# Optimization experiments

Measured on AMD Instinct MI355X. Metric: run time of the kernel, lower is better.

The kernel has to match this reference:

```python
import jax, jax.numpy as jnp
import numpy as np

B, T, I, H, S = 4096, 512, 4, 32, 4


def setup_inputs() -> dict:
    key = jax.random.key(0)
    ks = jax.random.split(key, 8)
    sc_ih = 1.0 / np.sqrt(H)
    return {
        "x": jax.random.normal(ks[0], (B, T, I), dtype=jnp.float32),
        "h0": jnp.zeros((1, B, H), dtype=jnp.float32),
        # PyTorch GRU params: weight_ih_l0 [3H, I] (r,z,n order), weight_hh_l0 [3H, H], biases [3H]
        "w_ih": jax.random.uniform(ks[1], (3 * H, I), jnp.float32, -sc_ih, sc_ih),
        "w_hh": jax.random.uniform(ks[2], (3 * H, H), jnp.float32, -sc_ih, sc_ih),
        "b_ih": jax.random.uniform(ks[3], (3 * H,), jnp.float32, -sc_ih, sc_ih),
        "b_hh": jax.random.uniform(ks[4], (3 * H,), jnp.float32, -sc_ih, sc_ih),
        "w_proj": jax.random.uniform(ks[5], (S, H), jnp.float32, -sc_ih, sc_ih),
        "b_proj": jax.random.uniform(ks[6], (S,), jnp.float32, -sc_ih, sc_ih),
    }


def _gru(x, h0, w_ih, w_hh, b_ih, b_hh):
    # Precompute input contributions for all timesteps: [B, T, 3H]
    xg = jnp.einsum('bti,gi->btg', x, w_ih) + b_ih
    xg_t = jnp.transpose(xg, (1, 0, 2))  # [T, B, 3H]
    h = h0[0]  # [B, H] (num_layers == 1)
    Hdim = w_hh.shape[1]

    def step(h, xg_step):
        hg = h @ w_hh.T + b_hh  # [B, 3H]
        xr, xz, xn = jnp.split(xg_step, 3, axis=-1)
        hr, hz, hn = jnp.split(hg, 3, axis=-1)
        r = jax.nn.sigmoid(xr + hr)
        z = jax.nn.sigmoid(xz + hz)
        n = jnp.tanh(xn + r * hn)
        h_new = (1.0 - z) * n + z * h
        return h_new, h_new

    hT, outs = jax.lax.scan(step, h, xg_t)
    out = jnp.transpose(outs, (1, 0, 2))  # [B, T, H]
    return out, hT[None]  # hn: [1, B, H]


def reference(x, h0, w_ih, w_hh, b_ih, b_hh, w_proj, b_proj):
    out, hn = _gru(x, h0, w_ih, w_hh, b_ih, b_hh)
    state = jnp.einsum('bth,sh->bts', out, w_proj) + b_proj  # [B, T, S]
    return state, hn
```

## Files before the change

kernel.cpp:

```cpp
#include <hip/hip_runtime.h>
#include <stdint.h>

#define BB 4096
#define TT 512
#define II 4
#define HH 32
#define SS 4

__device__ __forceinline__ float fast_sigm(float a) {
  return __builtin_amdgcn_rcpf(1.0f + __expf(-a));
}
__device__ __forceinline__ float fast_tanh(float y) {
  return 1.0f - 2.0f * __builtin_amdgcn_rcpf(__expf(2.0f * y) + 1.0f);
}

__global__ __launch_bounds__(256, 2) void gru_kernel(
    const float* __restrict__ x, const float* __restrict__ h0,
    const float* __restrict__ w_ih, const float* __restrict__ w_hh,
    const float* __restrict__ b_ih, const float* __restrict__ b_hh,
    const float* __restrict__ w_proj, const float* __restrict__ b_proj,
    float* __restrict__ out) {
  const int tid  = threadIdx.x;
  const int wid  = tid >> 6;
  const int lane = tid & 63;
  const int g    = lane >> 5;
  const int j    = lane & 31;
  const int row  = wid * 2 + g;
  const int b    = blockIdx.x * 8 + row;

  __shared__ float lds_h[8][36];
  float* lrow = &lds_h[row][0];

  const float4* whh4 = (const float4*)w_hh;
  float4 wr[8], wz[8], wn[8];
#pragma unroll
  for (int c = 0; c < 8; ++c) {
    wr[c] = whh4[(0 * HH + j) * 8 + c];
    wz[c] = whh4[(1 * HH + j) * 8 + c];
    wn[c] = whh4[(2 * HH + j) * 8 + c];
  }
  const float4* wih4 = (const float4*)w_ih;
  const float4 wir = wih4[0 * HH + j];
  const float4 wiz = wih4[1 * HH + j];
  const float4 win = wih4[2 * HH + j];
  const float bir = b_ih[0 * HH + j], biz = b_ih[1 * HH + j], bin_ = b_ih[2 * HH + j];
  const float bhr = b_hh[0 * HH + j], bhz = b_hh[1 * HH + j], bhn = b_hh[2 * HH + j];

  const int s_idx = j & 3;
  const int c_idx = j >> 2;
  const float4* wp4 = (const float4*)w_proj;
  const float4 wp = wp4[s_idx * 8 + c_idx];
  const float bp = b_proj[s_idx];

  float h_self = h0[(size_t)b * HH + j];
  lrow[j] = h_self;

  const float4* xp = (const float4*)(x + (size_t)b * TT * II);
  float* outp = out + (size_t)b * TT * SS;

  float4 xv = xp[0];

  for (int t = 0; t < TT; ++t) {
    float4 xvn = xp[(t + 1 < TT) ? (t + 1) : t];

    float4 ha[8];
#pragma unroll
    for (int c = 0; c < 8; ++c) ha[c] = *(const float4*)&lrow[c * 4];

    float xr = fmaf(wir.x, xv.x, fmaf(wir.y, xv.y, fmaf(wir.z, xv.z, fmaf(wir.w, xv.w, bir))));
    float xz = fmaf(wiz.x, xv.x, fmaf(wiz.y, xv.y, fmaf(wiz.z, xv.z, fmaf(wiz.w, xv.w, biz))));
    float xn = fmaf(win.x, xv.x, fmaf(win.y, xv.y, fmaf(win.z, xv.z, fmaf(win.w, xv.w, bin_))));

    float hr = bhr, hz = bhz, hn = bhn;
#pragma unroll
    for (int c = 0; c < 8; ++c) {
      hr = fmaf(wr[c].x, ha[c].x, hr); hr = fmaf(wr[c].y, ha[c].y, hr);
      hr = fmaf(wr[c].z, ha[c].z, hr); hr = fmaf(wr[c].w, ha[c].w, hr);
      hz = fmaf(wz[c].x, ha[c].x, hz); hz = fmaf(wz[c].y, ha[c].y, hz);
      hz = fmaf(wz[c].z, ha[c].z, hz); hz = fmaf(wz[c].w, ha[c].w, hz);
      hn = fmaf(wn[c].x, ha[c].x, hn); hn = fmaf(wn[c].y, ha[c].y, hn);
      hn = fmaf(wn[c].z, ha[c].z, hn); hn = fmaf(wn[c].w, ha[c].w, hn);
    }

    const float r  = fast_sigm(xr + hr);
    const float zz = fast_sigm(xz + hz);
    const float nn = fast_tanh(fmaf(r, hn, xn));
    const float hnew = fmaf(zz, h_self - nn, nn);
    h_self = hnew;

    lrow[j] = hnew;

    const float4 hc = *(const float4*)&lrow[c_idx * 4];
    float v = fmaf(wp.x, hc.x, fmaf(wp.y, hc.y, fmaf(wp.z, hc.z, wp.w * hc.w)));
    v += __shfl_xor(v, 4, 64);
    v += __shfl_xor(v, 8, 64);
    v += __shfl_xor(v, 16, 64);
    if (c_idx == 0) {
      outp[t * SS + s_idx] = v + bp;
    }

    xv = xvn;
  }

  out[(size_t)BB * TT * SS + (size_t)b * HH + j] = h_self;
}

extern "C" void kernel_launch(void* const* d_in, const int* in_sizes, int n_in,
                              void* d_out, int out_size, void* d_ws, size_t ws_size,
                              hipStream_t stream) {
  const float* x      = (const float*)d_in[0];
  const float* h0     = (const float*)d_in[1];
  const float* w_ih   = (const float*)d_in[2];
  const float* w_hh   = (const float*)d_in[3];
  const float* b_ih   = (const float*)d_in[4];
  const float* b_hh   = (const float*)d_in[5];
  const float* w_proj = (const float*)d_in[6];
  const float* b_proj = (const float*)d_in[7];
  float* out = (float*)d_out;

  dim3 grid(BB / 8), block(256);
  hipLaunchKernelGGL(gru_kernel, grid, block, 0, stream,
                     x, h0, w_ih, w_hh, b_ih, b_hh, w_proj, b_proj, out);
}
```

Baseline: 332.5 us.

## Split GRU hidden dot product across wave halves with packed FMA

Each wavefront now handles one batch row instead of two. Each half-wave computes half of the 32-wide recurrent dot product using v_pk_fma_f32, and the halves are combined with a cross-half shuffle. This halves the per-thread weight registers and serial FMA chain, and launch bounds rise to 4 blocks per CU for more occupancy. The projection output is moved to the start of the next iteration so it overlaps with the recurrence. The trade-off is twice as many blocks and redundant gate math in both halves.

Result: slower. 361.1 us (+8.6%).

```diff
diff --git a/kernel.cpp b/kernel.cpp
--- a/kernel.cpp
+++ b/kernel.cpp
@@ -3,9 +3,10 @@
 
 #define BB 4096
 #define TT 512
-#define II 4
 #define HH 32
 #define SS 4
+
+typedef float v2f __attribute__((ext_vector_type(2)));
 
 __device__ __forceinline__ float fast_sigm(float a) {
   return __builtin_amdgcn_rcpf(1.0f + __expf(-a));
@@ -13,8 +14,12 @@
 __device__ __forceinline__ float fast_tanh(float y) {
   return 1.0f - 2.0f * __builtin_amdgcn_rcpf(__expf(2.0f * y) + 1.0f);
 }
+__device__ __forceinline__ v2f pkfma(v2f a, v2f b, v2f c) {
+  asm("v_pk_fma_f32 %0, %1, %2, %0" : "+v"(c) : "v"(a), "v"(b));
+  return c;
+}
 
-__global__ __launch_bounds__(256, 2) void gru_kernel(
+__global__ __launch_bounds__(256, 4) void gru_kernel(
     const float* __restrict__ x, const float* __restrict__ h0,
     const float* __restrict__ w_ih, const float* __restrict__ w_hh,
     const float* __restrict__ b_ih, const float* __restrict__ b_hh,
@@ -23,28 +28,36 @@
   const int tid  = threadIdx.x;
   const int wid  = tid >> 6;
   const int lane = tid & 63;
-  const int g    = lane >> 5;
   const int j    = lane & 31;
-  const int row  = wid * 2 + g;
-  const int b    = blockIdx.x * 8 + row;
+  const int half = lane >> 5;
+  const int b    = blockIdx.x * 4 + wid;
 
-  __shared__ float lds_h[8][36];
-  float* lrow = &lds_h[row][0];
+  __shared__ float lds_h[4][36];
+  float* lrow = &lds_h[wid][0];
 
   const float4* whh4 = (const float4*)w_hh;
-  float4 wr[8], wz[8], wn[8];
+  v2f wr2[8], wz2[8], wn2[8];
 #pragma unroll
-  for (int c = 0; c < 8; ++c) {
-    wr[c] = whh4[(0 * HH + j) * 8 + c];
-    wz[c] = whh4[(1 * HH + j) * 8 + c];
-    wn[c] = whh4[(2 * HH + j) * 8 + c];
+  for (int c = 0; c < 4; ++c) {
+    float4 q;
+    q = whh4[(0 * HH + j) * 8 + half * 4 + c];
+    wr2[2*c] = (v2f){q.x, q.y}; wr2[2*c+1] = (v2f){q.z, q.w};
+    q = whh4[(1 * HH + j) * 8 + half * 4 + c];
+    wz2[2*c] = (v2f){q.x, q.y}; wz2[2*c+1] = (v2f){q.z, q.w};
+    q = whh4[(2 * HH + j) * 8 + half * 4 + c];
+    wn2[2*c] = (v2f){q.x, q.y}; wn2[2*c+1] = (v2f){q.z, q.w};
   }
+#pragma unroll
+  for (int m = 0; m < 8; ++m) {
+    asm("" : "+v"(wr2[m]), "+v"(wz2[m]), "+v"(wn2[m]));
+  }
+
   const float4* wih4 = (const float4*)w_ih;
   const float4 wir = wih4[0 * HH + j];
   const float4 wiz = wih4[1 * HH + j];
   const float4 win = wih4[2 * HH + j];
-  const float bir = b_ih[0 * HH + j], biz = b_ih[1 * HH + j], bin_ = b_ih[2 * HH + j];
-  const float bhr = b_hh[0 * HH + j], bhz = b_hh[1 * HH + j], bhn = b_hh[2 * HH + j];
+  const float bir = b_ih[0*HH + j], biz = b_ih[1*HH + j], bin_ = b_ih[2*HH + j];
+  const float bhr = b_hh[0*HH + j], bhz = b_hh[1*HH + j], bhn = b_hh[2*HH + j];
 
   const int s_idx = j & 3;
   const int c_idx = j >> 2;
@@ -55,32 +68,49 @@
   float h_self = h0[(size_t)b * HH + j];
   lrow[j] = h_self;
 
-  const float4* xp = (const float4*)(x + (size_t)b * TT * II);
+  const float4* xp = (const float4*)(x + (size_t)b * TT * 4);
   float* outp = out + (size_t)b * TT * SS;
+  const float* hk_addr = lrow + half * 16;
+  const float* hc_addr = lrow + (c_idx << 2);
 
-  float4 xv = xp[0];
+  for (int t = 0; t <= TT; ++t) {
+    v2f h2[8];
+#pragma unroll
+    for (int c = 0; c < 4; ++c) {
+      const float4 q = *(const float4*)(hk_addr + 4 * c);
+      h2[2*c] = (v2f){q.x, q.y}; h2[2*c+1] = (v2f){q.z, q.w};
+    }
+    const float4 hcv = *(const float4*)hc_addr;
 
-  for (int t = 0; t < TT; ++t) {
-    float4 xvn = xp[(t + 1 < TT) ? (t + 1) : t];
+    if (t > 0) {
+      float v = fmaf(wp.x, hcv.x, fmaf(wp.y, hcv.y,
+                fmaf(wp.z, hcv.z, wp.w * hcv.w)));
+      v += __shfl_xor(v, 4, 64);
+      v += __shfl_xor(v, 8, 64);
+      v += __shfl_xor(v, 16, 64);
+      if (lane < 4) {
+        outp[(t - 1) * SS + lane] = v + bp;
+      }
+    }
+    if (t == TT) break;
 
-    float4 ha[8];
-#pragma unroll
-    for (int c = 0; c < 8; ++c) ha[c] = *(const float4*)&lrow[c * 4];
+    const float4 xv = xp[t];
 
     float xr = fmaf(wir.x, xv.x, fmaf(wir.y, xv.y, fmaf(wir.z, xv.z, fmaf(wir.w, xv.w, bir))));
     float xz = fmaf(wiz.x, xv.x, fmaf(wiz.y, xv.y, fmaf(wiz.z, xv.z, fmaf(wiz.w, xv.w, biz))));
     float xn = fmaf(win.x, xv.x, fmaf(win.y, xv.y, fmaf(win.z, xv.z, fmaf(win.w, xv.w, bin_))));
 
-    float hr = bhr, hz = bhz, hn = bhn;
+    v2f aR = (v2f){0.f, 0.f}, aZ = (v2f){0.f, 0.f}, aN = (v2f){0.f, 0.f};
 #pragma unroll
-    for (int c = 0; c < 8; ++c) {
-      hr = fmaf(wr[c].x, ha[c].x, hr); hr = fmaf(wr[c].y, ha[c].y, hr);
-      hr = fmaf(wr[c].z, ha[c].z, hr); hr = fmaf(wr[c].w, ha[c].w, hr);
-      hz = fmaf(wz[c].x, ha[c].x, hz); hz = fmaf(wz[c].y, ha[c].y, hz);
-      hz = fmaf(wz[c].z, ha[c].z, hz); hz = fmaf(wz[c].w, ha[c].w, hz);
-      hn = fmaf(wn[c].x, ha[c].x, hn); hn = fmaf(wn[c].y, ha[c].y, hn);
-      hn = fmaf(wn[c].z, ha[c].z, hn); hn = fmaf(wn[c].w, ha[c].w, hn);
+    for (int m = 0; m < 8; ++m) {
+      aR = pkfma(wr2[m], h2[m], aR);
+      aZ = pkfma(wz2[m], h2[m], aZ);
+      aN = pkfma(wn2[m], h2[m], aN);
     }
+    float hrp = aR.x + aR.y, hzp = aZ.x + aZ.y, hnp = aN.x + aN.y;
+    const float hr = hrp + __shfl_xor(hrp, 32, 64) + bhr;
+    const float hz = hzp + __shfl_xor(hzp, 32, 64) + bhz;
+    const float hn = hnp + __shfl_xor(hnp, 32, 64) + bhn;
 
     const float r  = fast_sigm(xr + hr);
     const float zz = fast_sigm(xz + hz);
@@ -89,20 +119,11 @@
     h_self = hnew;
 
     lrow[j] = hnew;
-
-    const float4 hc = *(const float4*)&lrow[c_idx * 4];
-    float v = fmaf(wp.x, hc.x, fmaf(wp.y, hc.y, fmaf(wp.z, hc.z, wp.w * hc.w)));
-    v += __shfl_xor(v, 4, 64);
-    v += __shfl_xor(v, 8, 64);
-    v += __shfl_xor(v, 16, 64);
-    if (c_idx == 0) {
-      outp[t * SS + s_idx] = v + bp;
-    }
-
-    xv = xvn;
   }
 
-  out[(size_t)BB * TT * SS + (size_t)b * HH + j] = h_self;
+  if (half == 0) {
+    out[(size_t)BB * TT * SS + (size_t)b * HH + j] = h_self;
+  }
 }
 
 extern "C" void kernel_launch(void* const* d_in, const int* in_sizes, int n_in,
@@ -118,7 +139,7 @@
   const float* b_proj = (const float*)d_in[7];
   float* out = (float*)d_out;
 
-  dim3 grid(BB / 8), block(256);
+  dim3 grid(BB / 4), block(256);
   hipLaunchKernelGGL(gru_kernel, grid, block, 0, stream,
                      x, h0, w_ih, w_hh, b_ih, b_hh, w_proj, b_proj, out);
 }
```

## Use packed FMA for hidden matvec and defer projection by one step

Applied to the files above, without the earlier changes.

Replaces the scalar FMA chains in the recurrent matvec with v_pk_fma_f32 on float pairs, which halves the FMA instruction count and splits each dot product into two accumulators. The projection of h_t is moved to the start of the next iteration so it shares the LDS read of the hidden state and sits off the recurrence's critical path. Weights are loaded with inline-asm global loads behind a single wait. The inline asm and sched barrier may constrain compiler scheduling, and the loop gains one extra iteration.

After: 291.9 us. 12.2% less time.

```diff
diff --git a/kernel.cpp b/kernel.cpp
--- a/kernel.cpp
+++ b/kernel.cpp
@@ -3,15 +3,29 @@
 
 #define BB 4096
 #define TT 512
-#define II 4
 #define HH 32
 #define SS 4
+
+typedef float v2f __attribute__((ext_vector_type(2)));
+
+#define STR2(x) #x
+#define STR(x) STR2(x)
+#define GLOAD4(dst, ptr, off)                                                  \
+  asm volatile("global_load_dwordx4 %0, %1, off offset:" STR(off)              \
+               : "=v"(dst) : "v"(ptr))
+#define GLOAD1(dst, ptr, off)                                                  \
+  asm volatile("global_load_dword %0, %1, off offset:" STR(off)                \
+               : "=v"(dst) : "v"(ptr))
 
 __device__ __forceinline__ float fast_sigm(float a) {
   return __builtin_amdgcn_rcpf(1.0f + __expf(-a));
 }
 __device__ __forceinline__ float fast_tanh(float y) {
   return 1.0f - 2.0f * __builtin_amdgcn_rcpf(__expf(2.0f * y) + 1.0f);
+}
+__device__ __forceinline__ v2f pkfma(v2f a, v2f b, v2f c) {
+  asm("v_pk_fma_f32 %0, %1, %2, %0" : "+v"(c) : "v"(a), "v"(b));
+  return c;
 }
 
 __global__ __launch_bounds__(256, 2) void gru_kernel(
@@ -31,56 +45,97 @@
   __shared__ float lds_h[8][36];
   float* lrow = &lds_h[row][0];
 
-  const float4* whh4 = (const float4*)w_hh;
-  float4 wr[8], wz[8], wn[8];
+  const int s_idx = j & 3;
+  const int c_idx = j >> 2;
+
+  float4 wq[24];
+  float4 wih_r, wih_z, wih_n;
+  float4 wp;
+  float bir, biz, bin_, bhr, bhz, bhn, bp;
+  {
+    const char* p0 = (const char*)(w_hh + (0 * HH + j) * HH);
+    const char* p1 = (const char*)(w_hh + (1 * HH + j) * HH);
+    const char* p2 = (const char*)(w_hh + (2 * HH + j) * HH);
+    GLOAD4(wq[0],  p0, 0);  GLOAD4(wq[1],  p0, 16);
+    GLOAD4(wq[2],  p0, 32); GLOAD4(wq[3],  p0, 48);
+    GLOAD4(wq[4],  p0, 64); GLOAD4(wq[5],  p0, 80);
+    GLOAD4(wq[6],  p0, 96); GLOAD4(wq[7],  p0, 112);
+    GLOAD4(wq[8],  p1, 0);  GLOAD4(wq[9],  p1, 16);
+    GLOAD4(wq[10], p1, 32); GLOAD4(wq[11], p1, 48);
+    GLOAD4(wq[12], p1, 64); GLOAD4(wq[13], p1, 80);
+    GLOAD4(wq[14], p1, 96); GLOAD4(wq[15], p1, 112);
+    GLOAD4(wq[16], p2, 0);  GLOAD4(wq[17], p2, 16);
+    GLOAD4(wq[18], p2, 32); GLOAD4(wq[19], p2, 48);
+    GLOAD4(wq[20], p2, 64); GLOAD4(wq[21], p2, 80);
+    GLOAD4(wq[22], p2, 96); GLOAD4(wq[23], p2, 112);
+    const char* pi = (const char*)(w_ih + j * 4);
+    GLOAD4(wih_r, pi, 0); GLOAD4(wih_z, pi, 512); GLOAD4(wih_n, pi, 1024);
+    const char* pbi = (const char*)(b_ih + j);
+    GLOAD1(bir, pbi, 0); GLOAD1(biz, pbi, 128); GLOAD1(bin_, pbi, 256);
+    const char* pbh = (const char*)(b_hh + j);
+    GLOAD1(bhr, pbh, 0); GLOAD1(bhz, pbh, 128); GLOAD1(bhn, pbh, 256);
+    const char* pp = (const char*)(w_proj + (s_idx * 8 + c_idx) * 4);
+    GLOAD4(wp, pp, 0);
+    const char* pbp = (const char*)(b_proj + s_idx);
+    GLOAD1(bp, pbp, 0);
+    asm volatile("s_waitcnt vmcnt(0)" ::: "memory");
+    __builtin_amdgcn_sched_barrier(0);
+  }
+
+  v2f wr2[16], wz2[16], wn2[16];
 #pragma unroll
   for (int c = 0; c < 8; ++c) {
-    wr[c] = whh4[(0 * HH + j) * 8 + c];
-    wz[c] = whh4[(1 * HH + j) * 8 + c];
-    wn[c] = whh4[(2 * HH + j) * 8 + c];
+    wr2[2*c] = (v2f){wq[c].x,    wq[c].y};    wr2[2*c+1] = (v2f){wq[c].z,    wq[c].w};
+    wz2[2*c] = (v2f){wq[8+c].x,  wq[8+c].y};  wz2[2*c+1] = (v2f){wq[8+c].z,  wq[8+c].w};
+    wn2[2*c] = (v2f){wq[16+c].x, wq[16+c].y}; wn2[2*c+1] = (v2f){wq[16+c].z, wq[16+c].w};
   }
-  const float4* wih4 = (const float4*)w_ih;
-  const float4 wir = wih4[0 * HH + j];
-  const float4 wiz = wih4[1 * HH + j];
-  const float4 win = wih4[2 * HH + j];
-  const float bir = b_ih[0 * HH + j], biz = b_ih[1 * HH + j], bin_ = b_ih[2 * HH + j];
-  const float bhr = b_hh[0 * HH + j], bhz = b_hh[1 * HH + j], bhn = b_hh[2 * HH + j];
-
-  const int s_idx = j & 3;
-  const int c_idx = j >> 2;
-  const float4* wp4 = (const float4*)w_proj;
-  const float4 wp = wp4[s_idx * 8 + c_idx];
-  const float bp = b_proj[s_idx];
 
   float h_self = h0[(size_t)b * HH + j];
   lrow[j] = h_self;
 
-  const float4* xp = (const float4*)(x + (size_t)b * TT * II);
+  const float4* xp = (const float4*)(x + (size_t)b * TT * 4);
   float* outp = out + (size_t)b * TT * SS;
+  const float* hc_addr = lrow + (c_idx << 2);
 
   float4 xv = xp[0];
 
-  for (int t = 0; t < TT; ++t) {
+  for (int t = 0; t <= TT; ++t) {
+    v2f h2[16];
+#pragma unroll
+    for (int c = 0; c < 8; ++c) {
+      const float4 q = *(const float4*)(lrow + 4 * c);
+      h2[2*c] = (v2f){q.x, q.y}; h2[2*c+1] = (v2f){q.z, q.w};
+    }
+    const float4 hcv = *(const float4*)hc_addr;
+
+    if (t > 0) {
+      float v = fmaf(wp.x, hcv.x, fmaf(wp.y, hcv.y,
+                fmaf(wp.z, hcv.z, wp.w * hcv.w)));
+      v += __shfl_xor(v, 4, 64);
+      v += __shfl_xor(v, 8, 64);
+      v += __shfl_xor(v, 16, 64);
+      if (c_idx == 0) {
+        outp[(t - 1) * SS + s_idx] = v + bp;
+      }
+    }
+    if (t == TT) break;
+
     float4 xvn = xp[(t + 1 < TT) ? (t + 1) : t];
 
-    float4 ha[8];
+    float xr = fmaf(wih_r.x, xv.x, fmaf(wih_r.y, xv.y, fmaf(wih_r.z, xv.z, fmaf(wih_r.w, xv.w, bir))));
+    float xz = fmaf(wih_z.x, xv.x, fmaf(wih_z.y, xv.y, fmaf(wih_z.z, xv.z, fmaf(wih_z.w, xv.w, biz))));
+    float xn = fmaf(wih_n.x, xv.x, fmaf(wih_n.y, xv.y, fmaf(wih_n.z, xv.z, fmaf(wih_n.w, xv.w, bin_))));
+
+    v2f aR = (v2f){bhr, 0.f}, aZ = (v2f){bhz, 0.f}, aN = (v2f){bhn, 0.f};
 #pragma unroll
-    for (int c = 0; c < 8; ++c) ha[c] = *(const float4*)&lrow[c * 4];
-
-    float xr = fmaf(wir.x, xv.x, fmaf(wir.y, xv.y, fmaf(wir.z, xv.z, fmaf(wir.w, xv.w, bir))));
-    float xz = fmaf(wiz.x, xv.x, fmaf(wiz.y, xv.y, fmaf(wiz.z, xv.z, fmaf(wiz.w, xv.w, biz))));
-    float xn = fmaf(win.x, xv.x, fmaf(win.y, xv.y, fmaf(win.z, xv.z, fmaf(win.w, xv.w, bin_))));
-
-    float hr = bhr, hz = bhz, hn = bhn;
-#pragma unroll
-    for (int c = 0; c < 8; ++c) {
-      hr = fmaf(wr[c].x, ha[c].x, hr); hr = fmaf(wr[c].y, ha[c].y, hr);
-      hr = fmaf(wr[c].z, ha[c].z, hr); hr = fmaf(wr[c].w, ha[c].w, hr);
-      hz = fmaf(wz[c].x, ha[c].x, hz); hz = fmaf(wz[c].y, ha[c].y, hz);
-      hz = fmaf(wz[c].z, ha[c].z, hz); hz = fmaf(wz[c].w, ha[c].w, hz);
-      hn = fmaf(wn[c].x, ha[c].x, hn); hn = fmaf(wn[c].y, ha[c].y, hn);
-      hn = fmaf(wn[c].z, ha[c].z, hn); hn = fmaf(wn[c].w, ha[c].w, hn);
+    for (int m = 0; m < 16; ++m) {
+      aR = pkfma(wr2[m], h2[m], aR);
+      aZ = pkfma(wz2[m], h2[m], aZ);
+      aN = pkfma(wn2[m], h2[m], aN);
     }
+    const float hr = aR.x + aR.y;
+    const float hz = aZ.x + aZ.y;
+    const float hn = aN.x + aN.y;
 
     const float r  = fast_sigm(xr + hr);
     const float zz = fast_sigm(xz + hz);
@@ -89,15 +144,6 @@
     h_self = hnew;
 
     lrow[j] = hnew;
-
-    const float4 hc = *(const float4*)&lrow[c_idx * 4];
-    float v = fmaf(wp.x, hc.x, fmaf(wp.y, hc.y, fmaf(wp.z, hc.z, wp.w * hc.w)));
-    v += __shfl_xor(v, 4, 64);
-    v += __shfl_xor(v, 8, 64);
-    v += __shfl_xor(v, 16, 64);
-    if (c_idx == 0) {
-      outp[t * SS + s_idx] = v + bp;
-    }
 
     xv = xvn;
   }
```

## Compute GRU recurrent matmul with bf16 MFMA using hi/lo split of hidden state

Applied to the files above, without the earlier changes.

Each 64-lane block now processes 16 batch rows and computes the hidden-to-hidden gates and the output projection with 16x16x32 bf16 MFMA instructions. The hidden state is split into a high and a low bf16 part so precision stays close to fp32, while the weights are rounded to bf16 only once. This replaces the per-lane 96-FMA scalar dot products and the shuffle reduction for the projection. It also double-buffers x in LDS and delays each projection store by one step. The cost is more MFMA issue per step and bf16 rounding error in the weights.

Result: slower. 476.2 us (+43.2%).

```diff
diff --git a/kernel.cpp b/kernel.cpp
--- a/kernel.cpp
+++ b/kernel.cpp
@@ -3,106 +3,184 @@
 
 #define BB 4096
 #define TT 512
-#define II 4
 #define HH 32
 #define SS 4
 
+typedef __attribute__((ext_vector_type(8))) short bf16x8;
+typedef __attribute__((ext_vector_type(4))) float f32x4;
+
+union Frag { uint32_t u[4]; bf16x8 v; };
+
+__device__ __forceinline__ uint32_t cvtpk(float a, float b) {
+  uint32_t d;
+  asm("v_cvt_pk_bf16_f32 %0, %1, %2" : "=v"(d) : "v"(a), "v"(b));
+  return d;
+}
+__device__ __forceinline__ float bflo(uint32_t u) { return __uint_as_float(u << 16); }
+__device__ __forceinline__ float bfhi(uint32_t u) { return __uint_as_float(u & 0xFFFF0000u); }
+
 __device__ __forceinline__ float fast_sigm(float a) {
   return __builtin_amdgcn_rcpf(1.0f + __expf(-a));
 }
 __device__ __forceinline__ float fast_tanh(float y) {
   return 1.0f - 2.0f * __builtin_amdgcn_rcpf(__expf(2.0f * y) + 1.0f);
 }
-
-__global__ __launch_bounds__(256, 2) void gru_kernel(
-    const float* __restrict__ x, const float* __restrict__ h0,
-    const float* __restrict__ w_ih, const float* __restrict__ w_hh,
-    const float* __restrict__ b_ih, const float* __restrict__ b_hh,
-    const float* __restrict__ w_proj, const float* __restrict__ b_proj,
-    float* __restrict__ out) {
-  const int tid  = threadIdx.x;
-  const int wid  = tid >> 6;
-  const int lane = tid & 63;
-  const int g    = lane >> 5;
-  const int j    = lane & 31;
-  const int row  = wid * 2 + g;
-  const int b    = blockIdx.x * 8 + row;
-
-  __shared__ float lds_h[8][36];
-  float* lrow = &lds_h[row][0];
-
-  const float4* whh4 = (const float4*)w_hh;
-  float4 wr[8], wz[8], wn[8];
-#pragma unroll
-  for (int c = 0; c < 8; ++c) {
-    wr[c] = whh4[(0 * HH + j) * 8 + c];
-    wz[c] = whh4[(1 * HH + j) * 8 + c];
-    wn[c] = whh4[(2 * HH + j) * 8 + c];
-  }
+__device__ __forceinline__ float dot4(float4 w, float4 x, float init) {
+  return fmaf(w.x, x.x, fmaf(w.y, x.y, fmaf(w.z, x.z, fmaf(w.w, x.w, init))));
+}
+
+#define MFMA(acc, afrag, bfrag) \
+  acc = __builtin_amdgcn_mfma_f32_16x16x32_bf16((afrag).v, (bfrag).v, acc, 0, 0, 0)
+
+#define MKB(frag, grow)                                                        \
+  { const float4* p_ = (const float4*)(w_hh + (size_t)(grow) * HH + k0);       \
+    float4 p0_ = p_[0], p1_ = p_[1];                                           \
+    (frag).u[0] = cvtpk(p0_.x, p0_.y); (frag).u[1] = cvtpk(p0_.z, p0_.w);      \
+    (frag).u[2] = cvtpk(p1_.x, p1_.y); (frag).u[3] = cvtpk(p1_.z, p1_.w); }
+
+__global__ void __attribute__((amdgpu_flat_work_group_size(64, 64)))
+__attribute__((amdgpu_waves_per_eu(1, 4)))
+gru_kernel(const float* __restrict__ x, const float* __restrict__ h0,
+           const float* __restrict__ w_ih, const float* __restrict__ w_hh,
+           const float* __restrict__ b_ih, const float* __restrict__ b_hh,
+           const float* __restrict__ w_proj, const float* __restrict__ b_proj,
+           float* __restrict__ out) {
+  const int lane = threadIdx.x;
+  const int c    = lane & 15;
+  const int qh   = lane >> 4;
+  const int k0   = qh * 8;
+  const int b0   = blockIdx.x * 16;
+
+  __shared__ float  hbuf[16][36];
+  __shared__ float4 xs[2][16];
+
+  {
+    const float4* hp = (const float4*)(h0 + (size_t)(b0 + c) * HH + k0);
+    float4 a0 = hp[0], a1 = hp[1];
+    *(float4*)&hbuf[c][k0]     = a0;
+    *(float4*)&hbuf[c][k0 + 4] = a1;
+  }
+  if (lane < 16) {
+    xs[0][lane] = *(const float4*)(x + (size_t)(b0 + lane) * TT * 4);
+  }
+
   const float4* wih4 = (const float4*)w_ih;
-  const float4 wir = wih4[0 * HH + j];
-  const float4 wiz = wih4[1 * HH + j];
-  const float4 win = wih4[2 * HH + j];
-  const float bir = b_ih[0 * HH + j], biz = b_ih[1 * HH + j], bin_ = b_ih[2 * HH + j];
-  const float bhr = b_hh[0 * HH + j], bhz = b_hh[1 * HH + j], bhn = b_hh[2 * HH + j];
-
-  const int s_idx = j & 3;
-  const int c_idx = j >> 2;
-  const float4* wp4 = (const float4*)w_proj;
-  const float4 wp = wp4[s_idx * 8 + c_idx];
-  const float bp = b_proj[s_idx];
-
-  float h_self = h0[(size_t)b * HH + j];
-  lrow[j] = h_self;
-
-  const float4* xp = (const float4*)(x + (size_t)b * TT * II);
-  float* outp = out + (size_t)b * TT * SS;
-
-  float4 xv = xp[0];
+  const float4 wr_c = wih4[c],      wr_d = wih4[16 + c];
+  const float4 wz_c = wih4[32 + c], wz_d = wih4[48 + c];
+  const float4 wn_c = wih4[64 + c], wn_d = wih4[80 + c];
+
+  const float bsr0 = b_ih[c]      + b_hh[c];
+  const float bsr1 = b_ih[16 + c] + b_hh[16 + c];
+  const float bsz0 = b_ih[32 + c] + b_hh[32 + c];
+  const float bsz1 = b_ih[48 + c] + b_hh[48 + c];
+  const float bin0 = b_ih[64 + c], bin1 = b_ih[80 + c];
+  const float bhn0 = b_hh[64 + c], bhn1 = b_hh[80 + c];
+  const float bp   = b_proj[c & 3];
+
+  Frag br0, br1, bz0, bz1, bn0, bn1, bpr;
+  MKB(br0, c);       MKB(br1, 16 + c);
+  MKB(bz0, 32 + c);  MKB(bz1, 48 + c);
+  MKB(bn0, 64 + c);  MKB(bn1, 80 + c);
+  if (c < 4) {
+    const float4* p = (const float4*)(w_proj + (size_t)c * HH + k0);
+    float4 p0 = p[0], p1 = p[1];
+    bpr.u[0] = cvtpk(p0.x, p0.y); bpr.u[1] = cvtpk(p0.z, p0.w);
+    bpr.u[2] = cvtpk(p1.x, p1.y); bpr.u[3] = cvtpk(p1.z, p1.w);
+  } else {
+    bpr.u[0] = 0; bpr.u[1] = 0; bpr.u[2] = 0; bpr.u[3] = 0;
+  }
 
   for (int t = 0; t < TT; ++t) {
-    float4 xvn = xp[(t + 1 < TT) ? (t + 1) : t];
-
-    float4 ha[8];
-#pragma unroll
-    for (int c = 0; c < 8; ++c) ha[c] = *(const float4*)&lrow[c * 4];
-
-    float xr = fmaf(wir.x, xv.x, fmaf(wir.y, xv.y, fmaf(wir.z, xv.z, fmaf(wir.w, xv.w, bir))));
-    float xz = fmaf(wiz.x, xv.x, fmaf(wiz.y, xv.y, fmaf(wiz.z, xv.z, fmaf(wiz.w, xv.w, biz))));
-    float xn = fmaf(win.x, xv.x, fmaf(win.y, xv.y, fmaf(win.z, xv.z, fmaf(win.w, xv.w, bin_))));
-
-    float hr = bhr, hz = bhz, hn = bhn;
-#pragma unroll
-    for (int c = 0; c < 8; ++c) {
-      hr = fmaf(wr[c].x, ha[c].x, hr); hr = fmaf(wr[c].y, ha[c].y, hr);
-      hr = fmaf(wr[c].z, ha[c].z, hr); hr = fmaf(wr[c].w, ha[c].w, hr);
-      hz = fmaf(wz[c].x, ha[c].x, hz); hz = fmaf(wz[c].y, ha[c].y, hz);
-      hz = fmaf(wz[c].z, ha[c].z, hz); hz = fmaf(wz[c].w, ha[c].w, hz);
-      hn = fmaf(wn[c].x, ha[c].x, hn); hn = fmaf(wn[c].y, ha[c].y, hn);
-      hn = fmaf(wn[c].z, ha[c].z, hn); hn = fmaf(wn[c].w, ha[c].w, hn);
-    }
-
-    const float r  = fast_sigm(xr + hr);
-    const float zz = fast_sigm(xz + hz);
-    const float nn = fast_tanh(fmaf(r, hn, xn));
-    const float hnew = fmaf(zz, h_self - nn, nn);
-    h_self = hnew;
-
-    lrow[j] = hnew;
-
-    const float4 hc = *(const float4*)&lrow[c_idx * 4];
-    float v = fmaf(wp.x, hc.x, fmaf(wp.y, hc.y, fmaf(wp.z, hc.z, wp.w * hc.w)));
-    v += __shfl_xor(v, 4, 64);
-    v += __shfl_xor(v, 8, 64);
-    v += __shfl_xor(v, 16, 64);
-    if (c_idx == 0) {
-      outp[t * SS + s_idx] = v + bp;
-    }
-
-    xv = xvn;
-  }
-
-  out[(size_t)BB * TT * SS + (size_t)b * HH + j] = h_self;
+    const int tn = (t + 1 < TT) ? (t + 1) : t;
+    float4 xpre;
+    if (lane < 16) {
+      xpre = *(const float4*)(x + (size_t)(b0 + lane) * TT * 4 + (size_t)tn * 4);
+    }
+
+    const float4 q0 = *(const float4*)&hbuf[c][k0];
+    const float4 q1 = *(const float4*)&hbuf[c][k0 + 4];
+    Frag ahi, alo;
+    ahi.u[0] = cvtpk(q0.x, q0.y); ahi.u[1] = cvtpk(q0.z, q0.w);
+    ahi.u[2] = cvtpk(q1.x, q1.y); ahi.u[3] = cvtpk(q1.z, q1.w);
+    alo.u[0] = cvtpk(q0.x - bflo(ahi.u[0]), q0.y - bfhi(ahi.u[0]));
+    alo.u[1] = cvtpk(q0.z - bflo(ahi.u[1]), q0.w - bfhi(ahi.u[1]));
+    alo.u[2] = cvtpk(q1.x - bflo(ahi.u[2]), q1.y - bfhi(ahi.u[2]));
+    alo.u[3] = cvtpk(q1.z - bflo(ahi.u[3]), q1.w - bfhi(ahi.u[3]));
+
+    f32x4 ar0, ar1, az0, az1, an0, an1, ap;
+    float xn0[4], xn1[4], hold0[4], hold1[4];
+#pragma unroll
+    for (int i = 0; i < 4; ++i) {
+      const int m = qh * 4 + i;
+      const float4 xv = xs[t & 1][m];
+      ar0[i] = dot4(wr_c, xv, bsr0);
+      ar1[i] = dot4(wr_d, xv, bsr1);
+      az0[i] = dot4(wz_c, xv, bsz0);
+      az1[i] = dot4(wz_d, xv, bsz1);
+      xn0[i] = dot4(wn_c, xv, bin0);
+      xn1[i] = dot4(wn_d, xv, bin1);
+      an0[i] = bhn0;
+      an1[i] = bhn1;
+      ap[i]  = 0.0f;
+      hold0[i] = hbuf[m][c];
+      hold1[i] = hbuf[m][16 + c];
+    }
+
+    MFMA(ar0, ahi, br0); MFMA(ar0, alo, br0);
+    MFMA(ar1, ahi, br1); MFMA(ar1, alo, br1);
+    MFMA(az0, ahi, bz0); MFMA(az0, alo, bz0);
+    MFMA(az1, ahi, bz1); MFMA(az1, alo, bz1);
+    MFMA(an0, ahi, bn0); MFMA(an0, alo, bn0);
+    MFMA(an1, ahi, bn1); MFMA(an1, alo, bn1);
+    MFMA(ap,  ahi, bpr); MFMA(ap,  alo, bpr);
+
+    if (lane < 16) xs[(t + 1) & 1][lane] = xpre;
+
+    if (t > 0 && c < 4) {
+#pragma unroll
+      for (int i = 0; i < 4; ++i) {
+        const int m = qh * 4 + i;
+        out[(size_t)(b0 + m) * TT * SS + (size_t)(t - 1) * SS + c] = ap[i] + bp;
+      }
+    }
+
+#pragma unroll
+    for (int i = 0; i < 4; ++i) {
+      const int m = qh * 4 + i;
+      const float r0 = fast_sigm(ar0[i]);
+      const float z0 = fast_sigm(az0[i]);
+      const float n0 = fast_tanh(fmaf(r0, an0[i], xn0[i]));
+      hbuf[m][c] = fmaf(z0, hold0[i] - n0, n0);
+      const float r1 = fast_sigm(ar1[i]);
+      const float z1 = fast_sigm(az1[i]);
+      const float n1 = fast_tanh(fmaf(r1, an1[i], xn1[i]));
+      hbuf[m][16 + c] = fmaf(z1, hold1[i] - n1, n1);
+    }
+  }
+
+  {
+    const float4 q0 = *(const float4*)&hbuf[c][k0];
+    const float4 q1 = *(const float4*)&hbuf[c][k0 + 4];
+    Frag ahi, alo;
+    ahi.u[0] = cvtpk(q0.x, q0.y); ahi.u[1] = cvtpk(q0.z, q0.w);
+    ahi.u[2] = cvtpk(q1.x, q1.y); ahi.u[3] = cvtpk(q1.z, q1.w);
+    alo.u[0] = cvtpk(q0.x - bflo(ahi.u[0]), q0.y - bfhi(ahi.u[0]));
+    alo.u[1] = cvtpk(q0.z - bflo(ahi.u[1]), q0.w - bfhi(ahi.u[1]));
+    alo.u[2] = cvtpk(q1.x - bflo(ahi.u[2]), q1.y - bfhi(ahi.u[2]));
+    alo.u[3] = cvtpk(q1.z - bflo(ahi.u[3]), q1.w - bfhi(ahi.u[3]));
+    f32x4 ap = {0.f, 0.f, 0.f, 0.f};
+    MFMA(ap, ahi, bpr); MFMA(ap, alo, bpr);
+    if (c < 4) {
+#pragma unroll
+      for (int i = 0; i < 4; ++i) {
+        const int m = qh * 4 + i;
+        out[(size_t)(b0 + m) * TT * SS + (size_t)(TT - 1) * SS + c] = ap[i] + bp;
+      }
+    }
+    float* hnp = out + (size_t)BB * TT * SS + (size_t)(b0 + c) * HH + k0;
+    *(float4*)hnp       = q0;
+    *(float4*)(hnp + 4) = q1;
+  }
 }
 
 extern "C" void kernel_launch(void* const* d_in, const int* in_sizes, int n_in,
@@ -118,7 +196,7 @@
   const float* b_proj = (const float*)d_in[7];
   float* out = (float*)d_out;
 
-  dim3 grid(BB / 8), block(256);
+  dim3 grid(BB / 16), block(64);
   hipLaunchKernelGGL(gru_kernel, grid, block, 0, stream,
                      x, h0, w_ih, w_hh, b_ih, b_hh, w_proj, b_proj, out);
 }
```
